# Performance work log

Hardware: AMD Instinct MI355X
Metric: run time of the kernel (lower is better)

The kernel has to match this reference:

```python
import jax, jax.numpy as jnp
import numpy as np

N = 4096      # vertices (ring graph)
R = 3         # ring connectivity radius -> n = 2R+1 = 7 neighbors (incl. self)
C0, C1, C2 = 16, 32, 32


def _build_graph():
    v = np.arange(N)

    def rfield(l):
        off = np.arange(-l * R, l * R + 1)
        return np.sort((v[:, None] + off[None, :]) % N, axis=1)  # [N, 2lR+1]

    rf0, rf1, rf2 = rfield(0), rfield(1), rfield(2)
    nbrs = rf1  # neighborhood(v, 1), sorted, includes v

    def chi_idx(rf_v, rf_prev):
        # position of each element of v's rfield inside each neighbor's prev rfield
        rfp = rf_prev[nbrs]                                   # [N, n, Kp]
        eq = rf_v[:, None, :, None] == rfp[:, :, None, :]     # [N, n, K, Kp]
        mask = eq.any(-1).astype(np.float32)                  # element present?
        idx = eq.argmax(-1).astype(np.int32)                  # gather index (0 if absent)
        return idx, mask

    idx1, mask1 = chi_idx(rf1, rf0)
    idx2, mask2 = chi_idx(rf2, rf1)

    def sub_adj(rf):
        d = np.abs(rf[:, :, None] - rf[:, None, :])
        d = np.minimum(d, N - d)
        return ((d >= 1) & (d <= R)).astype(np.float32)       # [N, K, K]

    return nbrs.astype(np.int32), idx1, mask1, idx2, mask2, sub_adj(rf1), sub_adj(rf2)


def setup_inputs() -> dict:
    key = jax.random.key(0)
    ks = jax.random.split(key, 10)
    nbrs, idx1, mask1, idx2, mask2, adj1, adj2 = _build_graph()
    return {
        "labels": jax.random.normal(ks[0], (N, C0), jnp.float32),
        "nbrs": jnp.asarray(nbrs),
        "idx1": jnp.asarray(idx1), "mask1": jnp.asarray(mask1),
        "idx2": jnp.asarray(idx2), "mask2": jnp.asarray(mask2),
        "adj1": jnp.asarray(adj1), "adj2": jnp.asarray(adj2),
        "W1": jax.random.normal(ks[1], (C1, C0), jnp.float32) * 0.1,
        "b1": jax.random.normal(ks[2], (C1,), jnp.float32) * 0.1,
        "W2": jax.random.normal(ks[3], (C2, C1), jnp.float32) * 0.1,
        "b2": jax.random.normal(ks[4], (C2,), jnp.float32) * 0.1,
        "al1": jax.random.normal(ks[5], (1,), jnp.float32),
        "al2": jax.random.normal(ks[6], (1,), jnp.float32),
        "Wfc": jax.random.normal(ks[7], (1, C2), jnp.float32) * 0.1,
        "bfc": jax.random.normal(ks[8], (1,), jnp.float32) * 0.1,
    }


def _level(feat_prev, nbrs, idx, mask, adj, al, W, b):
    # feat_prev: [N, C, Kp, Kp]; idx/mask: [N, n, K]; adj: [N, K, K]
    g = feat_prev[nbrs]                                          # [N, n, C, Kp, Kp]
    g = jnp.take_along_axis(g, idx[:, :, None, :, None], axis=3)  # [N, n, C, K, Kp]
    g = jnp.take_along_axis(g, idx[:, :, None, None, :], axis=4)  # [N, n, C, K, K]
    g = g * mask[:, :, None, :, None] * mask[:, :, None, None, :]  # chi F chi^T
    agg = g.sum(axis=1) + al * adj[:, None, :, :]                # [N, C, K, K]
    n_, C, K, _ = agg.shape
    x = agg.reshape(n_, K * K, C)            # faithful to torch .view(k*k, -1)
    y = jax.nn.relu(x @ W.T + b)             # [N, K*K, Cout]
    return y.reshape(n_, W.shape[0], K, K)   # faithful to torch .view(out, k, k)


def reference(labels, nbrs, idx1, mask1, idx2, mask2, adj1, adj2,
              W1, b1, W2, b2, al1, al2, Wfc, bfc):
    feat0 = labels.reshape(N, C0, 1, 1)
    f1 = _level(feat0, nbrs, idx1, mask1, adj1, al1, W1, b1)
    f2 = _level(f1, nbrs, idx2, mask2, adj2, al2, W2, b2)
    g_repr = f2.sum(axis=(2, 3)).sum(axis=0, keepdims=True)      # [1, C2]
    output = g_repr @ Wfc.T + bfc                                # [1, 1]
    return output, g_repr
```

## Files before the change

kernel.cpp:

```cpp
#include <hip/hip_runtime.h>

#define NV 4096
#define NMASK 4095
#define NN 7
#define KK1 49
#define KK2 169
#define C0 16
#define C1 32
#define C2 32
#define F1LEN 1568
#define RSTR 882
#define QSTR 18
#define VB 4
#define NB (NV / VB)
#define NT 704
#define WROWS 10
#define LROWS 16
#define TIL 31

typedef unsigned int uint;
typedef unsigned short ushort;
typedef unsigned char uchar;
typedef __attribute__((ext_vector_type(8))) short short8v;
typedef __attribute__((ext_vector_type(4))) float float4v;

static __device__ __forceinline__ ushort f2bf(float f) {
    union { float f; uint u; } v; v.f = f;
    uint r = (v.u + 0x7fffu + ((v.u >> 16) & 1u)) >> 16;
    return (ushort)r;
}
static __device__ __forceinline__ float bflo(uint w) { return __uint_as_float(w << 16); }
static __device__ __forceinline__ float bfhi(uint w) { return __uint_as_float(w & 0xffff0000u); }

struct PermT { ushort v[176]; };
static constexpr PermT make_perm() {
    PermT p{};
    int idx = 0;
    for (int c = 7; c >= 0; --c)
        for (int i = 0; i < 13; ++i)
            for (int j = 0; j < 13; ++j) {
                int mn = i < j ? i : j, mx = i < j ? j : i;
                int lo = (mx - 9 < -3) ? -3 : mx - 9;
                int hi = (mn - 3 > 3) ? 3 : mn - 3;
                int cnt = hi - lo + 1; if (cnt < 0) cnt = 0;
                if (cnt == c) { p.v[idx] = (ushort)((c << 8) | (i << 4) | j); ++idx; }
            }
    return p;
}
__device__ constexpr PermT PERM = make_perm();

__global__ __launch_bounds__(704) void fused_kernel(
    const float* __restrict__ labels, const int* __restrict__ nbrs,
    const float* __restrict__ mask1, const int* __restrict__ idx2,
    const float* __restrict__ mask2, const float* __restrict__ adj1,
    const float* __restrict__ adj2, const float* __restrict__ W1,
    const float* __restrict__ b1, const float* __restrict__ W2,
    const float* __restrict__ b2, const float* __restrict__ al1,
    const float* __restrict__ al2, float* __restrict__ gpart)
{
    __shared__ __align__(16) uint   fs[WROWS * RSTR];
    __shared__ __align__(16) ushort aggT[VB * 5408];
    __shared__ float m2s[VB][91];
    __shared__ uchar i2q[VB][96];
    __shared__ int   rowOf2[VB][NN];
    __shared__ float grs[32];
    __shared__ float al1s, al2s;

    float* aggf = (float*)aggT;
    float* Lw   = (float*)((char*)aggT + 31360);
    float* m1w  = (float*)((char*)aggT + 32384);
    int*   nbrW = (int*)  ((char*)aggT + 34344);

    int t = threadIdx.x;
    int v0 = blockIdx.x * VB;
    int lane = t & 63, wvid = t >> 6;
    int r16 = lane & 15, kg = lane >> 4;
    bool interior = (v0 >= 6) && (v0 + 9 <= NMASK);

    if (t < 32) grs[t] = 0.f;
    if (t == 0) { al1s = al1[0]; al2s = al2[0]; }
    for (int e = t; e < LROWS * 16; e += NT)
        Lw[e] = labels[(size_t)(((v0 - 6 + (e >> 4)) + NV) & NMASK) * 16 + (e & 15)];
    for (int e = t; e < WROWS * 49; e += NT)
        m1w[e] = mask1[(size_t)(((v0 - 3 + e / 49) + NV) & NMASK) * 49 + (e % 49)];
    for (int e = t; e < WROWS * NN; e += NT) {
        int r = e / NN, u = e % NN;
        nbrW[e] = (nbrs[(size_t)(((v0 - 3 + r) + NV) & NMASK) * NN + u] - v0 + 6 + NV) & NMASK;
    }
    if (!interior) {
        for (int e = t; e < VB * 91; e += NT) {
            int vl = e / 91, x = e % 91;
            m2s[vl][x] = mask2[(size_t)v0 * 91 + e];
            i2q[vl][x] = (uchar)idx2[(size_t)v0 * 91 + e];
        }
        for (int e = t; e < VB * NN; e += NT)
            rowOf2[e / NN][e % NN] = (nbrs[v0 * NN + e] - v0 + 3 + NV) & NMASK;
    }
    __syncthreads();

    if (t < WROWS * 49) {
        int r = t / 49, ij = t % 49, i = ij / 7, j = ij % 7;
        float a[16];
        #pragma unroll
        for (int c = 0; c < 16; ++c) a[c] = 0.f;
        #pragma unroll
        for (int u = 0; u < NN; ++u) {
            float mm = m1w[r * 49 + u * 7 + i] * m1w[r * 49 + u * 7 + j];
            const float4* lr = (const float4*)&Lw[nbrW[r * 7 + u] * 16];
            float4 l0 = lr[0], l1 = lr[1], l2 = lr[2], l3 = lr[3];
            a[0]+=mm*l0.x; a[1]+=mm*l0.y; a[2]+=mm*l0.z; a[3]+=mm*l0.w;
            a[4]+=mm*l1.x; a[5]+=mm*l1.y; a[6]+=mm*l1.z; a[7]+=mm*l1.w;
            a[8]+=mm*l2.x; a[9]+=mm*l2.y; a[10]+=mm*l2.z; a[11]+=mm*l2.w;
            a[12]+=mm*l3.x; a[13]+=mm*l3.y; a[14]+=mm*l3.z; a[15]+=mm*l3.w;
        }
        float av = al1s * adj1[(size_t)(((v0 - 3 + r) + NV) & NMASK) * 49 + ij];
        #pragma unroll
        for (int c = 0; c < 16; ++c)
            aggf[r * 784 + c * 49 + ij] = a[c] + av;
    }
    __syncthreads();

    {
        short8v wb0, wb1;
        #pragma unroll
        for (int e = 0; e < 8; ++e) {
            int k = kg * 8 + e;
            wb0[e] = (k < 16) ? (short)f2bf(W1[r16 * 16 + k]) : (short)0;
            wb1[e] = (k < 16) ? (short)f2bf(W1[(r16 + 16) * 16 + k]) : (short)0;
        }
        float bb0 = b1[r16], bb1 = b1[r16 + 16];
        ushort* fsh = (ushort*)fs;
        for (int tile = wvid; tile < TIL; tile += 11) {
            int m = tile * 16 + r16;
            short8v a;
            #pragma unroll
            for (int e = 0; e < 8; ++e) a[e] = 0;
            if (kg < 2 && m < WROWS * 49) {
                int r = m / 49, p = m % 49;
                const float4* xp = (const float4*)(aggf + r * 784 + p * 16 + kg * 8);
                float4 xa = xp[0], xb = xp[1];
                a[0]=(short)f2bf(xa.x); a[1]=(short)f2bf(xa.y); a[2]=(short)f2bf(xa.z); a[3]=(short)f2bf(xa.w);
                a[4]=(short)f2bf(xb.x); a[5]=(short)f2bf(xb.y); a[6]=(short)f2bf(xb.z); a[7]=(short)f2bf(xb.w);
            }
            float4v z = {0.f, 0.f, 0.f, 0.f};
            float4v d0 = __builtin_amdgcn_mfma_f32_16x16x32_bf16(a, wb0, z, 0, 0, 0);
            float4v d1 = __builtin_amdgcn_mfma_f32_16x16x32_bf16(a, wb1, z, 0, 0, 0);
            #pragma unroll
            for (int rr = 0; rr < 4; ++rr) {
                int m2 = tile * 16 + kg * 4 + rr;
                if (m2 < WROWS * 49) {
                    int r = m2 / 49, p = m2 % 49;
                    int f2a = p * 32 + r16;
                    int ca = f2a / 49, qa = f2a % 49;
                    int wa = (ca >> 1) ^ ((qa >> 4) << 1);
                    fsh[(r * RSTR + qa * QSTR + wa) * 2 + (ca & 1)] = f2bf(fmaxf(d0[rr] + bb0, 0.f));
                    int f2b = f2a + 16;
                    int cb = f2b / 49, qb = f2b % 49;
                    int wb = (cb >> 1) ^ ((qb >> 4) << 1);
                    fsh[(r * RSTR + qb * QSTR + wb) * 2 + (cb & 1)] = f2bf(fmaxf(d1[rr] + bb1, 0.f));
                }
            }
        }
    }
    __syncthreads();

    if (t < VB * KK2) {
        int vl = t & 3, s = t >> 2;
        uint cell = PERM.v[s];
        int i = (cell >> 4) & 15, j = cell & 15;
        int ij = i * 13 + j;
        int cnt, dlo;
        if (interior) {
            cnt = cell >> 8;
            int mn = i < j ? i : j, mx = i < j ? j : i;
            dlo = (mx - 9 < -3) ? -3 : mx - 9;
        } else { cnt = 7; dlo = 0; }
        float acc[32];
        #pragma unroll
        for (int c = 0; c < 32; ++c) acc[c] = 0.f;
        #pragma unroll
        for (int n = 0; n < 7; ++n) {
            if (n < cnt) {
                float mm; int q, row;
                if (interior) {
                    int d = dlo + n;
                    q = (i - 3 - d) * 7 + (j - 3 - d);
                    row = vl + 3 + d;
                    mm = 1.f;
                } else {
                    mm = m2s[vl][n * 13 + i] * m2s[vl][n * 13 + j];
                    q = (int)i2q[vl][n * 13 + i] * 7 + (int)i2q[vl][n * 13 + j];
                    row = rowOf2[vl][n];
                }
                const uint* base = fs + row * RSTR + q * QSTR;
                int sw = (q >> 4) << 1;
                #pragma unroll
                for (int e = 0; e < 8; ++e) {
                    uint2 dd = *(const uint2*)(base + ((2 * e) ^ sw));
                    acc[4*e+0] += mm * bflo(dd.x);
                    acc[4*e+1] += mm * bfhi(dd.x);
                    acc[4*e+2] += mm * bflo(dd.y);
                    acc[4*e+3] += mm * bfhi(dd.y);
                }
            }
        }
        float av;
        if (interior) {
            int adiff = i > j ? i - j : j - i;
            av = (adiff >= 1 && adiff <= 3) ? al2s : 0.f;
        } else {
            av = al2s * adj2[(size_t)(v0 + vl) * KK2 + ij];
        }
        #pragma unroll
        for (int c = 0; c < 32; ++c)
            aggT[vl * 5408 + c * KK2 + ij] = f2bf(acc[c] + av);
    }
    __syncthreads();

    {
        short8v cb0, cb1;
        #pragma unroll
        for (int e = 0; e < 8; ++e) {
            cb0[e] = (short)f2bf(W2[r16 * 32 + kg * 8 + e]);
            cb1[e] = (short)f2bf(W2[(r16 + 16) * 32 + kg * 8 + e]);
        }
        float bias0 = b2[r16], bias1 = b2[r16 + 16];
        int p0 = wvid * 16;
        int prow = p0 + r16; if (prow > 168) prow = 168;
        float s0[4] = {0.f,0.f,0.f,0.f}, s1[4] = {0.f,0.f,0.f,0.f};
        #pragma unroll
        for (int vl = 0; vl < VB; ++vl) {
            const uint4* ap = (const uint4*)((const char*)aggT + vl * 10816 + prow * 64 + kg * 16);
            uint4 araw = *ap;
            short8v a = *reinterpret_cast<short8v*>(&araw);
            float4v z = {0.f, 0.f, 0.f, 0.f};
            float4v d0 = __builtin_amdgcn_mfma_f32_16x16x32_bf16(a, cb0, z, 0, 0, 0);
            float4v d1 = __builtin_amdgcn_mfma_f32_16x16x32_bf16(a, cb1, z, 0, 0, 0);
            #pragma unroll
            for (int r = 0; r < 4; ++r) {
                s0[r] += fmaxf(d0[r] + bias0, 0.f);
                s1[r] += fmaxf(d1[r] + bias1, 0.f);
            }
        }
        int chA = (p0 * 32) / KK2;
        float part0 = 0.f, part1 = 0.f, part2 = 0.f, part3 = 0.f;
        #pragma unroll
        for (int r = 0; r < 4; ++r) {
            int p = p0 + kg * 4 + r;
            if (p < KK2) {
                int c0 = (p * 32 + r16) / KK2 - chA;
                part0 += (c0 == 0) ? s0[r] : 0.f;
                part1 += (c0 == 1) ? s0[r] : 0.f;
                part2 += (c0 == 2) ? s0[r] : 0.f;
                part3 += (c0 == 3) ? s0[r] : 0.f;
                int c1 = (p * 32 + r16 + 16) / KK2 - chA;
                part0 += (c1 == 0) ? s1[r] : 0.f;
                part1 += (c1 == 1) ? s1[r] : 0.f;
                part2 += (c1 == 2) ? s1[r] : 0.f;
                part3 += (c1 == 3) ? s1[r] : 0.f;
            }
        }
        #pragma unroll
        for (int off = 32; off > 0; off >>= 1) {
            part0 += __shfl_xor(part0, off);
            part1 += __shfl_xor(part1, off);
            part2 += __shfl_xor(part2, off);
            part3 += __shfl_xor(part3, off);
        }
        if (lane == 0) {
            atomicAdd(&grs[chA], part0);
            if (chA + 1 < 32) atomicAdd(&grs[chA + 1], part1);
            if (chA + 2 < 32) atomicAdd(&grs[chA + 2], part2);
            if (chA + 3 < 32) atomicAdd(&grs[chA + 3], part3);
        }
    }
    __syncthreads();
    if (t < 32) gpart[blockIdx.x * 32 + t] = grs[t];
}

__global__ __launch_bounds__(1024) void fc_kernel(
    const float* __restrict__ gpart, const float* __restrict__ Wfc,
    const float* __restrict__ bfc, float* __restrict__ out)
{
    __shared__ float red[32][33];
    int t = threadIdx.x;
    int ch = t & 31, seg = t >> 5;
    float s = 0.f;
    for (int b = seg; b < NB; b += 32) s += gpart[b * 32 + ch];
    red[seg][ch] = s;
    __syncthreads();
    if (t < 32) {
        float g = 0.f;
        #pragma unroll
        for (int k = 0; k < 32; ++k) g += red[k][t];
        out[1 + t] = g;
        red[0][t] = g * Wfc[t];
    }
    __syncthreads();
    if (t == 0) {
        float p = bfc[0];
        #pragma unroll
        for (int k = 0; k < 32; ++k) p += red[0][k];
        out[0] = p;
    }
}

__global__ __launch_bounds__(64) void lvl1_kernel(
    const float* __restrict__ labels, const int* __restrict__ nbrs,
    const float* __restrict__ mask1, const float* __restrict__ adj1,
    const float* __restrict__ W1, const float* __restrict__ b1,
    const float* __restrict__ al1, float* __restrict__ f1out)
{
    __shared__ float Ls[NN][C0];
    __shared__ float m1s[NN][7];
    __shared__ float a1s[KK1];
    __shared__ float aggsh[C0 * KK1];
    __shared__ float W1s[C1 * 17];
    __shared__ float b1s[C1];
    int v = blockIdx.x, t = threadIdx.x;
    for (int e = t; e < NN * C0; e += 64) {
        int u = e >> 4, c = e & 15;
        Ls[u][c] = labels[(size_t)nbrs[v * NN + u] * C0 + c];
    }
    for (int e = t; e < KK1; e += 64) {
        m1s[e / 7][e % 7] = mask1[(size_t)v * KK1 + e];
        a1s[e] = adj1[(size_t)v * KK1 + e];
    }
    for (int e = t; e < C1 * C0; e += 64) W1s[(e >> 4) * 17 + (e & 15)] = W1[e];
    if (t < C1) b1s[t] = b1[t];
    float alpha = al1[0];
    __syncthreads();
    for (int e = t; e < C0 * KK1; e += 64) {
        int c = e / KK1, ij = e % KK1, i = ij / 7, j = ij % 7;
        float s = 0.f;
        #pragma unroll
        for (int u = 0; u < NN; ++u) s += Ls[u][c] * (m1s[u][i] * m1s[u][j]);
        aggsh[e] = s + alpha * a1s[ij];
    }
    __syncthreads();
    int co = t & 31;
    for (int e = t; e < F1LEN; e += 64) {
        int p = e >> 5;
        float s = b1s[co];
        #pragma unroll
        for (int c = 0; c < C0; ++c) s += aggsh[p * C0 + c] * W1s[co * 17 + c];
        f1out[(size_t)v * F1LEN + e] = fmaxf(s, 0.f);
    }
}

#define F1PAD 56
#define AGPAD 177
__global__ __launch_bounds__(192) void lvl2_kernel(
    const float* __restrict__ f1, const int* __restrict__ nbrs,
    const int* __restrict__ idx2, const float* __restrict__ mask2,
    const float* __restrict__ adj2, const float* __restrict__ W2,
    const float* __restrict__ b2, const float* __restrict__ al2,
    float* __restrict__ gr)
{
    __shared__ float f1s[C1 * F1PAD];
    __shared__ float aggT2[C1 * AGPAD];
    __shared__ float W2s[C2 * C1];
    __shared__ float b2s[C2];
    __shared__ float grs[C2];
    __shared__ int nbs[NN];
    int v = blockIdx.x, t = threadIdx.x;
    if (t < NN) nbs[t] = nbrs[v * NN + t];
    if (t < C2) { b2s[t] = b2[t]; grs[t] = 0.f; }
    for (int e = t; e < C2 * C1; e += 192) W2s[e] = W2[e];
    float alpha = al2[0];
    bool act = (t < KK2);
    float mmr[NN]; int qr[NN];
    float acc[C1];
    if (act) {
        int i = t / 13, j = t % 13;
        const float* mbase = mask2 + (size_t)v * NN * 13;
        const int* ibase = idx2 + (size_t)v * NN * 13;
        #pragma unroll
        for (int u = 0; u < NN; ++u) {
            mmr[u] = mbase[u * 13 + i] * mbase[u * 13 + j];
            qr[u] = ibase[u * 13 + i] * 7 + ibase[u * 13 + j];
        }
    }
    #pragma unroll
    for (int c = 0; c < C1; ++c) acc[c] = 0.f;
    int dst[9]; int nd = 0;
    for (int e = t; e < F1LEN; e += 192) dst[nd++] = (e / 49) * F1PAD + (e % 49);
    for (int u = 0; u < NN; ++u) {
        __syncthreads();
        const float* src = f1 + (size_t)nbs[u] * F1LEN;
        { int k = 0; for (int e = t; e < F1LEN; e += 192) f1s[dst[k++]] = src[e]; }
        __syncthreads();
        if (act) {
            float mv = mmr[u]; int q = qr[u];
            #pragma unroll
            for (int c = 0; c < C1; ++c) acc[c] += mv * f1s[c * F1PAD + q];
        }
    }
    if (act) {
        float a2v = alpha * adj2[(size_t)v * KK2 + t];
        #pragma unroll
        for (int c = 0; c < C1; ++c) {
            int f = c * KK2 + t;
            aggT2[(f & 31) * AGPAD + (f >> 5)] = acc[c] + a2v;
        }
    }
    __syncthreads();
    if (act) {
        int p = t;
        float ar[C1];
        #pragma unroll
        for (int c2 = 0; c2 < C1; ++c2) ar[c2] = aggT2[c2 * AGPAD + p];
        int chA = (p * 32) / KK2;
        int csplit = KK2 - (p * 32 - chA * KK2);
        float sA = 0.f, sB = 0.f;
        #pragma unroll
        for (int co = 0; co < C2; ++co) {
            float s = b2s[co];
            #pragma unroll
            for (int k = 0; k < 8; ++k) {
                float4 wv = *(const float4*)(&W2s[co * C1 + 4 * k]);
                s += ar[4*k+0]*wv.x + ar[4*k+1]*wv.y + ar[4*k+2]*wv.z + ar[4*k+3]*wv.w;
            }
            s = fmaxf(s, 0.f);
            if (co < csplit) sA += s; else sB += s;
        }
        atomicAdd(&grs[chA], sA);
        if (csplit < 32) atomicAdd(&grs[chA + 1], sB);
    }
    __syncthreads();
    if (t < C2) atomicAdd(&gr[t], grs[t]);
}

__global__ __launch_bounds__(64) void fc_small_kernel(
    const float* __restrict__ gr, const float* __restrict__ Wfc,
    const float* __restrict__ bfc, float* __restrict__ out)
{
    int t = threadIdx.x;
    float g = (t < C2) ? gr[t] : 0.f;
    if (t < C2) out[1 + t] = g;
    float p = (t < C2) ? g * Wfc[t] : 0.f;
    #pragma unroll
    for (int off = 32; off > 0; off >>= 1) p += __shfl_down(p, off);
    if (t == 0) out[0] = p + bfc[0];
}

extern "C" void kernel_launch(void* const* d_in, const int* in_sizes, int n_in,
                              void* d_out, int out_size, void* d_ws, size_t ws_size,
                              hipStream_t stream)
{
    const float* labels = (const float*)d_in[0];
    const int*   nbrs   = (const int*)d_in[1];
    const float* mask1  = (const float*)d_in[3];
    const int*   idx2   = (const int*)d_in[4];
    const float* mask2  = (const float*)d_in[5];
    const float* adj1   = (const float*)d_in[6];
    const float* adj2   = (const float*)d_in[7];
    const float* W1     = (const float*)d_in[8];
    const float* b1     = (const float*)d_in[9];
    const float* W2     = (const float*)d_in[10];
    const float* b2     = (const float*)d_in[11];
    const float* al1    = (const float*)d_in[12];
    const float* al2    = (const float*)d_in[13];
    const float* Wfc    = (const float*)d_in[14];
    const float* bfc    = (const float*)d_in[15];

    if (ws_size >= (size_t)NB * 32 * sizeof(float)) {
        float* gpart = (float*)d_ws;
        fused_kernel<<<NB, NT, 0, stream>>>(labels, nbrs, mask1, idx2, mask2,
                                            adj1, adj2, W1, b1, W2, b2, al1, al2, gpart);
        fc_kernel<<<1, 1024, 0, stream>>>(gpart, Wfc, bfc, (float*)d_out);
    } else {
        float* f1 = (float*)d_ws;
        float* gr = (float*)((char*)d_ws + (size_t)NV * F1LEN * sizeof(float));
        hipMemsetAsync(gr, 0, C2 * sizeof(float), stream);
        lvl1_kernel<<<NV, 64, 0, stream>>>(labels, nbrs, mask1, adj1, W1, b1, al1, f1);
        lvl2_kernel<<<NV, 192, 0, stream>>>(f1, nbrs, idx2, mask2, adj2, W2, b2, al2, gr);
        fc_small_kernel<<<1, 64, 0, stream>>>(gr, Wfc, bfc, (float*)d_out);
    }
}
```

Measured before the change: 54.28 us.

## Specialize interior level-1 aggregation and restructure shared feature layout with LUT

For interior blocks, the level-1 aggregation is built directly from the closed form (a diagonal label value plus alpha on the ring band) stored as bf16. This skips the mask and neighbour gathers and the 7-neighbour accumulation. The level-1 feature scratch is relaid out as an unpadded bf16 row with a simple XOR swizzle. Write addresses come from a precomputed shared lookup table, and level-2 reads use 16-byte vector loads. The changes aim to cut integer division overhead, shared memory footprint and LDS load count, but the bf16 aggregate slightly changes rounding and the new swizzle may bring back bank conflicts.

Result: slower. 65.92 us (+21.4%).

```diff
diff --git a/kernel.cpp b/kernel.cpp
--- a/kernel.cpp
+++ b/kernel.cpp
@@ -9,14 +9,15 @@
 #define C1 32
 #define C2 32
 #define F1LEN 1568
-#define RSTR 882
-#define QSTR 18
 #define VB 4
 #define NB (NV / VB)
 #define NT 704
 #define WROWS 10
 #define LROWS 16
 #define TIL 31
+#define FSROW 1568
+#define FSROWW 784
+#define HALFW 392
 
 typedef unsigned int uint;
 typedef unsigned short ushort;
@@ -58,18 +59,19 @@
     const float* __restrict__ b2, const float* __restrict__ al1,
     const float* __restrict__ al2, float* __restrict__ gpart)
 {
-    __shared__ __align__(16) uint   fs[WROWS * RSTR];
+    __shared__ __align__(16) ushort fsh[WROWS * FSROW];
     __shared__ __align__(16) ushort aggT[VB * 5408];
+    __shared__ ushort lutg[F1LEN];
     __shared__ float m2s[VB][91];
     __shared__ uchar i2q[VB][96];
     __shared__ int   rowOf2[VB][NN];
     __shared__ float grs[32];
     __shared__ float al1s, al2s;
 
-    float* aggf = (float*)aggT;
-    float* Lw   = (float*)((char*)aggT + 31360);
-    float* m1w  = (float*)((char*)aggT + 32384);
-    int*   nbrW = (int*)  ((char*)aggT + 34344);
+    ushort* aggf16 = aggT;
+    float* Lw   = (float*)((char*)aggT + 15680);
+    float* m1w  = (float*)((char*)aggT + 16704);
+    int*   nbrW = (int*)  ((char*)aggT + 18664);
 
     int t = threadIdx.x;
     int v0 = blockIdx.x * VB;
@@ -81,13 +83,17 @@
     if (t == 0) { al1s = al1[0]; al2s = al2[0]; }
     for (int e = t; e < LROWS * 16; e += NT)
         Lw[e] = labels[(size_t)(((v0 - 6 + (e >> 4)) + NV) & NMASK) * 16 + (e & 15)];
-    for (int e = t; e < WROWS * 49; e += NT)
-        m1w[e] = mask1[(size_t)(((v0 - 3 + e / 49) + NV) & NMASK) * 49 + (e % 49)];
-    for (int e = t; e < WROWS * NN; e += NT) {
-        int r = e / NN, u = e % NN;
-        nbrW[e] = (nbrs[(size_t)(((v0 - 3 + r) + NV) & NMASK) * NN + u] - v0 + 6 + NV) & NMASK;
+    for (int e = t; e < F1LEN; e += NT) {
+        int c = e / 49, q = e - c * 49;
+        lutg[e] = (ushort)((c >> 4) * 784 + q * 16 + ((c & 15) ^ ((q & 1) << 3)));
     }
     if (!interior) {
+        for (int e = t; e < WROWS * 49; e += NT)
+            m1w[e] = mask1[(size_t)(((v0 - 3 + e / 49) + NV) & NMASK) * 49 + (e % 49)];
+        for (int e = t; e < WROWS * NN; e += NT) {
+            int r = e / NN, u = e % NN;
+            nbrW[e] = (nbrs[(size_t)(((v0 - 3 + r) + NV) & NMASK) * NN + u] - v0 + 6 + NV) & NMASK;
+        }
         for (int e = t; e < VB * 91; e += NT) {
             int vl = e / 91, x = e % 91;
             m2s[vl][x] = mask2[(size_t)v0 * 91 + e];
@@ -98,7 +104,24 @@
     }
     __syncthreads();
 
-    if (t < WROWS * 49) {
+    if (interior) {
+        ushort al1b = f2bf(al1s);
+        int e = t, fx = t, r = 0;
+        int c = t / 49;
+        int ij = t - c * 49;
+        int i = ij / 7;
+        int j = ij - i * 7;
+        while (e < WROWS * 784) {
+            int ad = i - j; ad = ad < 0 ? -ad : ad;
+            ushort lv = f2bf(Lw[(r + i) * 16 + c]);
+            ushort val = (ad == 0) ? lv : ((ad <= 3) ? al1b : (ushort)0);
+            aggf16[r * 784 + fx] = val;
+            e += NT; fx += NT; c += 14; ij += 18; i += 2; j += 4;
+            if (j >= 7) { j -= 7; i += 1; }
+            if (ij >= 49) { ij -= 49; c += 1; i -= 7; }
+            if (fx >= 784) { fx -= 784; c -= 16; r += 1; }
+        }
+    } else if (t < WROWS * 49) {
         int r = t / 49, ij = t % 49, i = ij / 7, j = ij % 7;
         float a[16];
         #pragma unroll
@@ -116,7 +139,7 @@
         float av = al1s * adj1[(size_t)(((v0 - 3 + r) + NV) & NMASK) * 49 + ij];
         #pragma unroll
         for (int c = 0; c < 16; ++c)
-            aggf[r * 784 + c * 49 + ij] = a[c] + av;
+            aggf16[r * 784 + c * 49 + ij] = f2bf(a[c] + av);
     }
     __syncthreads();
 
@@ -129,35 +152,27 @@
             wb1[e] = (k < 16) ? (short)f2bf(W1[(r16 + 16) * 16 + k]) : (short)0;
         }
         float bb0 = b1[r16], bb1 = b1[r16 + 16];
-        ushort* fsh = (ushort*)fs;
         for (int tile = wvid; tile < TIL; tile += 11) {
             int m = tile * 16 + r16;
             short8v a;
             #pragma unroll
             for (int e = 0; e < 8; ++e) a[e] = 0;
             if (kg < 2 && m < WROWS * 49) {
-                int r = m / 49, p = m % 49;
-                const float4* xp = (const float4*)(aggf + r * 784 + p * 16 + kg * 8);
-                float4 xa = xp[0], xb = xp[1];
-                a[0]=(short)f2bf(xa.x); a[1]=(short)f2bf(xa.y); a[2]=(short)f2bf(xa.z); a[3]=(short)f2bf(xa.w);
-                a[4]=(short)f2bf(xb.x); a[5]=(short)f2bf(xb.y); a[6]=(short)f2bf(xb.z); a[7]=(short)f2bf(xb.w);
+                int r = m / 49, p = m - r * 49;
+                uint4 araw = *(const uint4*)((const uint*)aggf16 + r * 392 + p * 8 + kg * 4);
+                a = *reinterpret_cast<short8v*>(&araw);
             }
             float4v z = {0.f, 0.f, 0.f, 0.f};
             float4v d0 = __builtin_amdgcn_mfma_f32_16x16x32_bf16(a, wb0, z, 0, 0, 0);
             float4v d1 = __builtin_amdgcn_mfma_f32_16x16x32_bf16(a, wb1, z, 0, 0, 0);
             #pragma unroll
             for (int rr = 0; rr < 4; ++rr) {
-                int m2 = tile * 16 + kg * 4 + rr;
-                if (m2 < WROWS * 49) {
-                    int r = m2 / 49, p = m2 % 49;
-                    int f2a = p * 32 + r16;
-                    int ca = f2a / 49, qa = f2a % 49;
-                    int wa = (ca >> 1) ^ ((qa >> 4) << 1);
-                    fsh[(r * RSTR + qa * QSTR + wa) * 2 + (ca & 1)] = f2bf(fmaxf(d0[rr] + bb0, 0.f));
-                    int f2b = f2a + 16;
-                    int cb = f2b / 49, qb = f2b % 49;
-                    int wb = (cb >> 1) ^ ((qb >> 4) << 1);
-                    fsh[(r * RSTR + qb * QSTR + wb) * 2 + (cb & 1)] = f2bf(fmaxf(d1[rr] + bb1, 0.f));
+                int m2v = tile * 16 + kg * 4 + rr;
+                if (m2v < WROWS * 49) {
+                    int r = m2v / 49, p = m2v - r * 49;
+                    int gb = p * 32 + r16;
+                    fsh[r * FSROW + lutg[gb]]      = f2bf(fmaxf(d0[rr] + bb0, 0.f));
+                    fsh[r * FSROW + lutg[gb + 16]] = f2bf(fmaxf(d1[rr] + bb1, 0.f));
                 }
             }
         }
@@ -169,47 +184,52 @@
         uint cell = PERM.v[s];
         int i = (cell >> 4) & 15, j = cell & 15;
         int ij = i * 13 + j;
-        int cnt, dlo;
+        float acc[32];
+        #pragma unroll
+        for (int c = 0; c < 32; ++c) acc[c] = 0.f;
+        const uint* fw = (const uint*)fsh;
+        float av;
+        int cnt, q0, row0;
         if (interior) {
             cnt = cell >> 8;
             int mn = i < j ? i : j, mx = i < j ? j : i;
-            dlo = (mx - 9 < -3) ? -3 : mx - 9;
-        } else { cnt = 7; dlo = 0; }
-        float acc[32];
-        #pragma unroll
-        for (int c = 0; c < 32; ++c) acc[c] = 0.f;
+            int dlo = (mx - 9 < -3) ? -3 : mx - 9;
+            q0 = (i - 3 - dlo) * 7 + (j - 3 - dlo);
+            row0 = vl + 3 + dlo;
+            int ad = i > j ? i - j : j - i;
+            av = (ad >= 1 && ad <= 3) ? al2s : 0.f;
+        } else {
+            cnt = 7; q0 = 0; row0 = 0;
+            av = al2s * adj2[(size_t)(v0 + vl) * KK2 + ij];
+        }
         #pragma unroll
         for (int n = 0; n < 7; ++n) {
             if (n < cnt) {
                 float mm; int q, row;
                 if (interior) {
-                    int d = dlo + n;
-                    q = (i - 3 - d) * 7 + (j - 3 - d);
-                    row = vl + 3 + d;
+                    q = q0 - 8 * n;
+                    row = row0 + n;
                     mm = 1.f;
                 } else {
                     mm = m2s[vl][n * 13 + i] * m2s[vl][n * 13 + j];
                     q = (int)i2q[vl][n * 13 + i] * 7 + (int)i2q[vl][n * 13 + j];
                     row = rowOf2[vl][n];
                 }
-                const uint* base = fs + row * RSTR + q * QSTR;
-                int sw = (q >> 4) << 1;
-                #pragma unroll
-                for (int e = 0; e < 8; ++e) {
-                    uint2 dd = *(const uint2*)(base + ((2 * e) ^ sw));
-                    acc[4*e+0] += mm * bflo(dd.x);
-                    acc[4*e+1] += mm * bfhi(dd.x);
-                    acc[4*e+2] += mm * bflo(dd.y);
-                    acc[4*e+3] += mm * bfhi(dd.y);
-                }
-            }
-        }
-        float av;
-        if (interior) {
-            int adiff = i > j ? i - j : j - i;
-            av = (adiff >= 1 && adiff <= 3) ? al2s : 0.f;
-        } else {
-            av = al2s * adj2[(size_t)(v0 + vl) * KK2 + ij];
+                int sw = (q & 1) << 2;
+                int base = row * FSROWW + (q << 3);
+                uint4 x0 = *(const uint4*)(fw + base + sw);
+                uint4 x1 = *(const uint4*)(fw + base + (sw ^ 4));
+                acc[0]+=mm*bflo(x0.x); acc[1]+=mm*bfhi(x0.x); acc[2]+=mm*bflo(x0.y); acc[3]+=mm*bfhi(x0.y);
+                acc[4]+=mm*bflo(x0.z); acc[5]+=mm*bfhi(x0.z); acc[6]+=mm*bflo(x0.w); acc[7]+=mm*bfhi(x0.w);
+                acc[8]+=mm*bflo(x1.x); acc[9]+=mm*bfhi(x1.x); acc[10]+=mm*bflo(x1.y); acc[11]+=mm*bfhi(x1.y);
+                acc[12]+=mm*bflo(x1.z); acc[13]+=mm*bfhi(x1.z); acc[14]+=mm*bflo(x1.w); acc[15]+=mm*bfhi(x1.w);
+                uint4 x2 = *(const uint4*)(fw + base + HALFW + sw);
+                uint4 x3 = *(const uint4*)(fw + base + HALFW + (sw ^ 4));
+                acc[16]+=mm*bflo(x2.x); acc[17]+=mm*bfhi(x2.x); acc[18]+=mm*bflo(x2.y); acc[19]+=mm*bfhi(x2.y);
+                acc[20]+=mm*bflo(x2.z); acc[21]+=mm*bfhi(x2.z); acc[22]+=mm*bflo(x2.w); acc[23]+=mm*bfhi(x2.w);
+                acc[24]+=mm*bflo(x3.x); acc[25]+=mm*bfhi(x3.x); acc[26]+=mm*bflo(x3.y); acc[27]+=mm*bfhi(x3.y);
+                acc[28]+=mm*bflo(x3.z); acc[29]+=mm*bfhi(x3.z); acc[30]+=mm*bflo(x3.w); acc[31]+=mm*bfhi(x3.w);
+            }
         }
         #pragma unroll
         for (int c = 0; c < 32; ++c)
@@ -230,8 +250,7 @@
         float s0[4] = {0.f,0.f,0.f,0.f}, s1[4] = {0.f,0.f,0.f,0.f};
         #pragma unroll
         for (int vl = 0; vl < VB; ++vl) {
-            const uint4* ap = (const uint4*)((const char*)aggT + vl * 10816 + prow * 64 + kg * 16);
-            uint4 araw = *ap;
+            uint4 araw = *(const uint4*)((const char*)aggT + vl * 10816 + prow * 64 + kg * 16);
             short8v a = *reinterpret_cast<short8v*>(&araw);
             float4v z = {0.f, 0.f, 0.f, 0.f};
             float4v d0 = __builtin_amdgcn_mfma_f32_16x16x32_bf16(a, cb0, z, 0, 0, 0);
```
